# Optimization experiments

Hardware: AMD Instinct MI355X
Metric: run time of the kernel (lower is better)

The kernel has to match this reference:

```python
import jax, jax.numpy as jnp
import numpy as np

MARGIN = 0.5
TIME_GAP = 10
EPS = 1e-8  # torch cosine_similarity eps


def setup_inputs() -> dict:
    key = jax.random.key(0)
    hidden_states = jax.random.normal(key, (16, 4096, 512), dtype=jnp.float32)
    return {"hidden_states": hidden_states}


def _sim_shift(h, n, k):
    # cosine similarity between time t and t+k for all valid t, all batches
    # h: [B, S, D], n: [B, S] precomputed norms -> returns [B, S-k]
    dots = jnp.sum(h[:, :-k] * h[:, k:], axis=-1)
    denom = jnp.maximum(n[:, :-k] * n[:, k:], EPS)
    return dots / denom


def reference(hidden_states):
    h = hidden_states
    B, S, D = h.shape
    n = jnp.sqrt(jnp.sum(h * h, axis=-1))  # [B, S], computed once

    # adjacent: sum_t mean_b(1 - sim(t, t+1)) / (S-1) == overall mean
    adjacent_loss = jnp.mean(1.0 - _sim_shift(h, n, 1))

    # distant: shifts k in [TIME_GAP, 2*TIME_GAP), t in [0, S-k)
    distant_total = jnp.zeros((), dtype=h.dtype)
    count = 0
    for k in range(TIME_GAP, min(S, 2 * TIME_GAP)):
        sim = _sim_shift(h, n, k)  # [B, S-k]
        # original sums mean-over-batch per (t,k) pair
        distant_total = distant_total + jnp.sum(jnp.mean(jax.nn.relu(MARGIN - sim), axis=0))
        count += S - k
    distant_loss = distant_total / count if count > 0 else jnp.zeros((), dtype=h.dtype)

    return adjacent_loss + distant_loss
```

## Files before the change

kernel.cpp:

```cpp
#include <hip/hip_runtime.h>
#include <math.h>

constexpr int B = 16;
constexpr int S = 4096;
constexpr int D = 512;
constexpr float MARGIN = 0.5f;
constexpr float EPS = 1e-8f;

constexpr int TG = 4;
constexpr int GROUPS_PER_BATCH = S / TG;
constexpr int TOTAL_WAVES = B * GROUPS_PER_BATCH;
constexpr int NBLOCKS = TOTAL_WAVES / 4;

__device__ inline float dot8(const float4& x0, const float4& x1,
                             const float4& y0, const float4& y1) {
    return x0.x * y0.x + x0.y * y0.y + x0.z * y0.z + x0.w * y0.w +
           x1.x * y1.x + x1.y * y1.y + x1.z * y1.z + x1.w * y1.w;
}

template <int CTRL>
__device__ __forceinline__ float dpp_add(float x) {
    int m = __builtin_amdgcn_update_dpp(0, __float_as_int(x), CTRL, 0xf, 0xf, true);
    return x + __int_as_float(m);
}

__device__ __forceinline__ float wave_sum63(float x) {
    x = dpp_add<0x111>(x);
    x = dpp_add<0x112>(x);
    x = dpp_add<0x114>(x);
    x = dpp_add<0x118>(x);
    x = dpp_add<0x142>(x);
    x = dpp_add<0x143>(x);
    return x;
}

__global__ __launch_bounds__(256, 2) void tcl_partial(const float* __restrict__ h,
                                                      float* __restrict__ ws) {
    const int lane  = threadIdx.x & 63;
    const int wslot = threadIdx.x >> 6;
    const int wid   = blockIdx.x * 4 + wslot;
    const int b     = wid >> 10;
    const int t0    = (wid & 1023) * TG;
    const float* base = h + (size_t)b * S * D + lane * 8;

    float4 a0[4], a1[4];
#pragma unroll
    for (int i = 0; i < 4; i++) {
        const float* q = base + (size_t)(t0 + i) * D;
        a0[i] = *(const float4*)q;
        a1[i] = *(const float4*)(q + 4);
    }
    float4 c0[14], c1[14];
#pragma unroll
    for (int j = 0; j < 14; j++) {
        const int off = (j == 0) ? 4 : (9 + j);
        const int s = t0 + off;
        c0[j] = make_float4(0.f, 0.f, 0.f, 0.f);
        c1[j] = make_float4(0.f, 0.f, 0.f, 0.f);
        if (s < S) {
            const float* q = base + (size_t)s * D;
            c0[j] = *(const float4*)q;
            c1[j] = *(const float4*)(q + 4);
        }
    }

    float n2o[4];
#pragma unroll
    for (int i = 0; i < 4; i++) n2o[i] = dot8(a0[i], a1[i], a0[i], a1[i]);

    float n2x[14];
#pragma unroll
    for (int j = 0; j < 14; j++) n2x[j] = dot8(c0[j], c1[j], c0[j], c1[j]);

    float dp[4][11];
#pragma unroll
    for (int i = 0; i < 4; i++)
#pragma unroll
        for (int q = 0; q < 11; q++) dp[i][q] = 0.f;

    dp[0][0] = dot8(a0[0], a1[0], a0[1], a1[1]);
    dp[1][0] = dot8(a0[1], a1[1], a0[2], a1[2]);
    dp[2][0] = dot8(a0[2], a1[2], a0[3], a1[3]);
    dp[3][0] = dot8(a0[3], a1[3], c0[0], c1[0]);

#pragma unroll
    for (int j = 1; j < 14; j++) {
#pragma unroll
        for (int i = 0; i < 4; i++) {
            const int k = 9 + j - i;
            if (k >= 10 && k <= 19)
                dp[i][k - 9] += dot8(a0[i], a1[i], c0[j], c1[j]);
        }
    }

#pragma unroll
    for (int i = 0; i < 4; i++) n2o[i] = wave_sum63(n2o[i]);
#pragma unroll
    for (int j = 0; j < 14; j++) n2x[j] = wave_sum63(n2x[j]);
#pragma unroll
    for (int i = 0; i < 4; i++)
#pragma unroll
        for (int q = 0; q < 11; q++) dp[i][q] = wave_sum63(dp[i][q]);

    float local = 0.f;
    if (lane == 63) {
        const float w1 = 1.0f / ((float)B * (float)(S - 1));
        const float w2 = 1.0f / ((float)B * (float)(10 * S - 145));
        float no[4];
#pragma unroll
        for (int i = 0; i < 4; i++) no[i] = sqrtf(n2o[i]);
        float nx[14];
#pragma unroll
        for (int j = 0; j < 14; j++) nx[j] = sqrtf(n2x[j]);

#pragma unroll
        for (int i = 0; i < 4; i++) {
            const int t = t0 + i;
            if (t + 1 < S) {
                const float nb = (i < 3) ? no[i + 1] : nx[0];
                const float sim = dp[i][0] / fmaxf(no[i] * nb, EPS);
                local += w1 * (1.0f - sim);
            }
#pragma unroll
            for (int k = 10; k <= 19; k++) {
                if (t + k < S) {
                    const float nb = nx[i + k - 9];
                    const float sim = dp[i][k - 9] / fmaxf(no[i] * nb, EPS);
                    const float r = MARGIN - sim;
                    local += w2 * (r > 0.f ? r : 0.f);
                }
            }
        }
    }

    __shared__ float bsum[4];
    if (lane == 63) bsum[wslot] = local;
    __syncthreads();
    if (threadIdx.x == 0)
        ws[blockIdx.x] = bsum[0] + bsum[1] + bsum[2] + bsum[3];
}

__global__ __launch_bounds__(1024) void tcl_final(const float* __restrict__ ws,
                                                  float* __restrict__ out) {
    float v = 0.f;
    for (int j = threadIdx.x; j < NBLOCKS; j += 1024) v += ws[j];
    v = wave_sum63(v);
    __shared__ float s[16];
    if ((threadIdx.x & 63) == 63) s[threadIdx.x >> 6] = v;
    __syncthreads();
    if (threadIdx.x == 0) {
        float t = 0.f;
#pragma unroll
        for (int j = 0; j < 16; j++) t += s[j];
        out[0] = t;
    }
}

extern "C" void kernel_launch(void* const* d_in, const int* in_sizes, int n_in,
                              void* d_out, int out_size, void* d_ws, size_t ws_size,
                              hipStream_t stream) {
    const float* h = (const float*)d_in[0];
    float* out = (float*)d_out;
    float* ws = (float*)d_ws;
    tcl_partial<<<NBLOCKS, 256, 0, stream>>>(h, ws);
    tcl_final<<<1, 1024, 0, stream>>>(ws, out);
}
```

Measured before the change: 208.6 us.

## Stage time-tile with halo in shared memory as truncated bf16 and widen per-wave rows

Each block now loads a 32-row tile plus a 19-row halo into LDS once, instead of every wave reloading its own 4 rows and 14 neighbour rows from global memory. This cuts redundant global/L2 traffic from about 4.5x the input to about 1.6x. Values are truncated to bf16 when stored in LDS, so the LDS footprint (~52KB) fits and fewer LDS bytes are read. The trade-off is lost precision in the dot products and norms relative to fp32, plus an extra barrier and more register pressure from 8 rows per wave.

```diff
diff --git a/kernel.cpp b/kernel.cpp
--- a/kernel.cpp
+++ b/kernel.cpp
@@ -7,23 +7,17 @@
 constexpr float MARGIN = 0.5f;
 constexpr float EPS = 1e-8f;
 
-constexpr int TG = 4;
-constexpr int GROUPS_PER_BATCH = S / TG;
-constexpr int TOTAL_WAVES = B * GROUPS_PER_BATCH;
-constexpr int NBLOCKS = TOTAL_WAVES / 4;
-
-__device__ inline float dot8(const float4& x0, const float4& x1,
-                             const float4& y0, const float4& y1) {
-    return x0.x * y0.x + x0.y * y0.y + x0.z * y0.z + x0.w * y0.w +
-           x1.x * y1.x + x1.y * y1.y + x1.z * y1.z + x1.w * y1.w;
-}
+constexpr int T  = 32;
+constexpr int TG = 8;
+constexpr int HALO = 19;
+constexpr int ROWS = T + HALO;
+constexpr int NBLK = B * (S / T);
 
 template <int CTRL>
 __device__ __forceinline__ float dpp_add(float x) {
     int m = __builtin_amdgcn_update_dpp(0, __float_as_int(x), CTRL, 0xf, 0xf, true);
     return x + __int_as_float(m);
 }
-
 __device__ __forceinline__ float wave_sum63(float x) {
     x = dpp_add<0x111>(x);
     x = dpp_add<0x112>(x);
@@ -34,98 +28,129 @@
     return x;
 }
 
+__device__ __forceinline__ void unpack8(const uint4& q, float* f) {
+    f[0] = __uint_as_float(q.x << 16);
+    f[1] = __uint_as_float(q.x & 0xffff0000u);
+    f[2] = __uint_as_float(q.y << 16);
+    f[3] = __uint_as_float(q.y & 0xffff0000u);
+    f[4] = __uint_as_float(q.z << 16);
+    f[5] = __uint_as_float(q.z & 0xffff0000u);
+    f[6] = __uint_as_float(q.w << 16);
+    f[7] = __uint_as_float(q.w & 0xffff0000u);
+}
+
+__device__ __forceinline__ float dot8f(const float* a, const float* b) {
+    float s = a[0] * b[0];
+#pragma unroll
+    for (int e = 1; e < 8; e++) s += a[e] * b[e];
+    return s;
+}
+
 __global__ __launch_bounds__(256, 2) void tcl_partial(const float* __restrict__ h,
                                                       float* __restrict__ ws) {
-    const int lane  = threadIdx.x & 63;
-    const int wslot = threadIdx.x >> 6;
-    const int wid   = blockIdx.x * 4 + wslot;
-    const int b     = wid >> 10;
-    const int t0    = (wid & 1023) * TG;
-    const float* base = h + (size_t)b * S * D + lane * 8;
+    __shared__ ushort sm[ROWS * D];
 
-    float4 a0[4], a1[4];
+    const int tid = threadIdx.x;
+    const int b   = blockIdx.x >> 7;
+    const int t0  = (blockIdx.x & 127) * T;
+    const float* base = h + (size_t)b * S * D;
+
 #pragma unroll
-    for (int i = 0; i < 4; i++) {
-        const float* q = base + (size_t)(t0 + i) * D;
-        a0[i] = *(const float4*)q;
-        a1[i] = *(const float4*)(q + 4);
-    }
-    float4 c0[14], c1[14];
-#pragma unroll
-    for (int j = 0; j < 14; j++) {
-        const int off = (j == 0) ? 4 : (9 + j);
-        const int s = t0 + off;
-        c0[j] = make_float4(0.f, 0.f, 0.f, 0.f);
-        c1[j] = make_float4(0.f, 0.f, 0.f, 0.f);
-        if (s < S) {
-            const float* q = base + (size_t)s * D;
-            c0[j] = *(const float4*)q;
-            c1[j] = *(const float4*)(q + 4);
+    for (int it = 0; it < 26; ++it) {
+        const int idx = tid + it * 256;
+        if (idx < ROWS * (D / 4)) {
+            const int r  = idx >> 7;
+            const int c4 = idx & 127;
+            const int t  = t0 + r;
+            float4 v = make_float4(0.f, 0.f, 0.f, 0.f);
+            if (t < S) v = *(const float4*)(base + (size_t)t * D + c4 * 4);
+            ushort4 u;
+            u.x = (ushort)(__float_as_uint(v.x) >> 16);
+            u.y = (ushort)(__float_as_uint(v.y) >> 16);
+            u.z = (ushort)(__float_as_uint(v.z) >> 16);
+            u.w = (ushort)(__float_as_uint(v.w) >> 16);
+            *(ushort4*)&sm[idx * 4] = u;
         }
     }
+    __syncthreads();
 
-    float n2o[4];
+    const int lane  = tid & 63;
+    const int w     = tid >> 6;
+    const int rbase = w * TG;
+
+    float ow[TG][8];
+    float n2o[TG];
 #pragma unroll
-    for (int i = 0; i < 4; i++) n2o[i] = dot8(a0[i], a1[i], a0[i], a1[i]);
+    for (int i = 0; i < TG; i++) {
+        uint4 q = *(const uint4*)&sm[(rbase + i) * D + lane * 8];
+        unpack8(q, ow[i]);
+        n2o[i] = dot8f(ow[i], ow[i]);
+    }
 
-    float n2x[14];
+    float dp1[TG];
 #pragma unroll
-    for (int j = 0; j < 14; j++) n2x[j] = dot8(c0[j], c1[j], c0[j], c1[j]);
+    for (int i = 0; i < TG - 1; i++) dp1[i] = dot8f(ow[i], ow[i + 1]);
 
-    float dp[4][11];
+    float dpd[TG][10];
 #pragma unroll
-    for (int i = 0; i < 4; i++)
+    for (int i = 0; i < TG; i++)
 #pragma unroll
-        for (int q = 0; q < 11; q++) dp[i][q] = 0.f;
+        for (int q = 0; q < 10; q++) dpd[i][q] = 0.f;
 
-    dp[0][0] = dot8(a0[0], a1[0], a0[1], a1[1]);
-    dp[1][0] = dot8(a0[1], a1[1], a0[2], a1[2]);
-    dp[2][0] = dot8(a0[2], a1[2], a0[3], a1[3]);
-    dp[3][0] = dot8(a0[3], a1[3], c0[0], c1[0]);
-
+    float n2x[18];
 #pragma unroll
-    for (int j = 1; j < 14; j++) {
+    for (int j = 0; j < 18; j++) {
+        const int off = (j == 0) ? TG : (9 + j);
+        uint4 q = *(const uint4*)&sm[(rbase + off) * D + lane * 8];
+        float cr[8];
+        unpack8(q, cr);
+        n2x[j] = dot8f(cr, cr);
+        if (j == 0) {
+            dp1[TG - 1] = dot8f(ow[TG - 1], cr);
+        } else {
 #pragma unroll
-        for (int i = 0; i < 4; i++) {
-            const int k = 9 + j - i;
-            if (k >= 10 && k <= 19)
-                dp[i][k - 9] += dot8(a0[i], a1[i], c0[j], c1[j]);
+            for (int i = 0; i < TG; i++) {
+                const int k = 9 + j - i;
+                if (k >= 10 && k <= 19) dpd[i][k - 10] += dot8f(ow[i], cr);
+            }
         }
     }
 
 #pragma unroll
-    for (int i = 0; i < 4; i++) n2o[i] = wave_sum63(n2o[i]);
+    for (int i = 0; i < TG; i++) n2o[i] = wave_sum63(n2o[i]);
 #pragma unroll
-    for (int j = 0; j < 14; j++) n2x[j] = wave_sum63(n2x[j]);
+    for (int i = 0; i < TG; i++) dp1[i] = wave_sum63(dp1[i]);
 #pragma unroll
-    for (int i = 0; i < 4; i++)
+    for (int j = 0; j < 18; j++) n2x[j] = wave_sum63(n2x[j]);
 #pragma unroll
-        for (int q = 0; q < 11; q++) dp[i][q] = wave_sum63(dp[i][q]);
+    for (int i = 0; i < TG; i++)
+#pragma unroll
+        for (int q = 0; q < 10; q++) dpd[i][q] = wave_sum63(dpd[i][q]);
 
     float local = 0.f;
     if (lane == 63) {
         const float w1 = 1.0f / ((float)B * (float)(S - 1));
         const float w2 = 1.0f / ((float)B * (float)(10 * S - 145));
-        float no[4];
+        float no[TG];
 #pragma unroll
-        for (int i = 0; i < 4; i++) no[i] = sqrtf(n2o[i]);
-        float nx[14];
+        for (int i = 0; i < TG; i++) no[i] = sqrtf(n2o[i]);
+        float nx[18];
 #pragma unroll
-        for (int j = 0; j < 14; j++) nx[j] = sqrtf(n2x[j]);
+        for (int j = 0; j < 18; j++) nx[j] = sqrtf(n2x[j]);
 
 #pragma unroll
-        for (int i = 0; i < 4; i++) {
-            const int t = t0 + i;
+        for (int i = 0; i < TG; i++) {
+            const int t = t0 + rbase + i;
             if (t + 1 < S) {
-                const float nb = (i < 3) ? no[i + 1] : nx[0];
-                const float sim = dp[i][0] / fmaxf(no[i] * nb, EPS);
+                const float nb = (i < TG - 1) ? no[i + 1] : nx[0];
+                const float sim = dp1[i] / fmaxf(no[i] * nb, EPS);
                 local += w1 * (1.0f - sim);
             }
 #pragma unroll
             for (int k = 10; k <= 19; k++) {
                 if (t + k < S) {
                     const float nb = nx[i + k - 9];
-                    const float sim = dp[i][k - 9] / fmaxf(no[i] * nb, EPS);
+                    const float sim = dpd[i][k - 10] / fmaxf(no[i] * nb, EPS);
                     const float r = MARGIN - sim;
                     local += w2 * (r > 0.f ? r : 0.f);
                 }
@@ -134,16 +159,15 @@
     }
 
     __shared__ float bsum[4];
-    if (lane == 63) bsum[wslot] = local;
+    if (lane == 63) bsum[w] = local;
     __syncthreads();
-    if (threadIdx.x == 0)
-        ws[blockIdx.x] = bsum[0] + bsum[1] + bsum[2] + bsum[3];
+    if (tid == 0) ws[blockIdx.x] = bsum[0] + bsum[1] + bsum[2] + bsum[3];
 }
 
 __global__ __launch_bounds__(1024) void tcl_final(const float* __restrict__ ws,
                                                   float* __restrict__ out) {
     float v = 0.f;
-    for (int j = threadIdx.x; j < NBLOCKS; j += 1024) v += ws[j];
+    for (int j = threadIdx.x; j < NBLK; j += 1024) v += ws[j];
     v = wave_sum63(v);
     __shared__ float s[16];
     if ((threadIdx.x & 63) == 63) s[threadIdx.x >> 6] = v;
@@ -162,6 +186,6 @@
     const float* h = (const float*)d_in[0];
     float* out = (float*)d_out;
     float* ws = (float*)d_ws;
-    tcl_partial<<<NBLOCKS, 256, 0, stream>>>(h, ws);
+    tcl_partial<<<NBLK, 256, 0, stream>>>(h, ws);
     tcl_final<<<1, 1024, 0, stream>>>(ws, out);
 }
```

Result: slower. 247.3 us (+18.5%).
